# Kernel optimization log

Measured on AMD Instinct MI355X. Metric: run time of the kernel, lower is better.

The kernel has to match this reference:

```python
import jax, jax.numpy as jnp
import numpy as np

B, S, R = 8192, 256, 8192  # gas cells, species, reactions


def setup_inputs() -> dict:
    key = jax.random.key(0)
    ks = jax.random.split(key, 10)
    abundances = jax.random.uniform(ks[0], (B, S), jnp.float32, 1e-12, 1.0)
    temperature = jax.random.uniform(ks[1], (B,), jnp.float32, 10.0, 300.0)
    cr_rate = jax.random.uniform(ks[2], (B,), jnp.float32, 0.1, 10.0)
    fuv_rate = jax.random.uniform(ks[3], (B,), jnp.float32, 0.1, 10.0)
    time = jnp.zeros((B,), jnp.float32)  # unused by the RHS, kept for signature parity
    incidence = jax.random.normal(ks[4], (S, R), jnp.float32)  # stoichiometry matrix
    alpha = jax.random.uniform(ks[5], (R,), jnp.float32, 1e-12, 1e-9)
    beta = jax.random.normal(ks[6], (R,), jnp.float32) * 0.5
    gamma = jax.random.uniform(ks[7], (R,), jnp.float32, 0.0, 100.0)
    # species index or S (== out-of-bounds sentinel -> fill_value 1.0, i.e. <2 reactants)
    reactant_multipliers = jax.random.randint(ks[8], (R, 2), 0, S + 1, jnp.int32)
    rtype = jax.random.randint(ks[9], (R,), 0, 3, jnp.int32)  # 0: Arrhenius, 1: CR, 2: FUV
    return {
        'time': time, 'abundances': abundances, 'temperature': temperature,
        'cr_rate': cr_rate, 'fuv_rate': fuv_rate, 'incidence': incidence,
        'alpha': alpha, 'beta': beta, 'gamma': gamma,
        'reactant_multipliers': reactant_multipliers, 'rtype': rtype,
    }


def _get_rates(temperature, cr_rate, fuv_rate, alpha, beta, gamma, rtype):
    # JNetwork.get_rates: hstack of per-reaction rate terms -> (B, R)
    T = temperature[:, None]                                      # (B, 1)
    k_arr = alpha * jnp.exp(beta * jnp.log(T / 300.0) - gamma / T)  # Arrhenius
    k_cr = alpha * cr_rate[:, None]                               # cosmic-ray driven
    k_fuv = alpha * jnp.exp(-gamma) * fuv_rate[:, None]           # FUV photorate
    return jnp.where(rtype == 0, k_arr, jnp.where(rtype == 1, k_cr, k_fuv))


def reference(time, abundances, temperature, cr_rate, fuv_rate,
              incidence, alpha, beta, gamma, reactant_multipliers, rtype):
    rates = _get_rates(temperature, cr_rate, fuv_rate, alpha, beta, gamma, rtype)
    # multiply_rates_by_abundance: gather reactant abundances (mode='drop',
    # fill_value=1.0) and reduce with a product over the 2 reactant slots.
    ones_col = jnp.ones((abundances.shape[0], 1), abundances.dtype)
    ab_pad = jnp.concatenate([abundances, ones_col], axis=1)      # (B, S+1), col S == 1.0
    prod = ab_pad[:, reactant_multipliers[:, 0]] * ab_pad[:, reactant_multipliers[:, 1]]  # (B, R)
    flux = rates * prod                                           # (B, R)
    # incidence @ rates, batched: (S, R) x (B, R) -> (B, S)
    return jnp.einsum('sr,br->bs', incidence, flux)
```

## Files before the change

kernel.cpp:

```cpp
#include <hip/hip_runtime.h>
#include <stdint.h>

typedef __bf16 bf16;
typedef __bf16 bf16x8 __attribute__((ext_vector_type(8)));
typedef float  f32x4  __attribute__((ext_vector_type(4)));

#if __has_builtin(__builtin_amdgcn_exp2f)
#define EXP2F(x) __builtin_amdgcn_exp2f(x)
#else
#define EXP2F(x) exp2f(x)
#endif

#define LGKM_BARRIER()                                    \
  do {                                                    \
    asm volatile("s_waitcnt lgkmcnt(0)" ::: "memory");    \
    __builtin_amdgcn_s_barrier();                         \
  } while (0)

constexpr int Bn = 8192, Sn = 256, Rn = 8192;
constexpr int BM = 64, BK = 32, KP = 4;
constexpr int KLEN = Rn / KP;
constexpr int NC = KLEN / BK;

__global__ __launch_bounds__(256) void prep_all(
    const float* __restrict__ inc, bf16* __restrict__ incb,
    const float* __restrict__ alpha, const float* __restrict__ beta,
    const float* __restrict__ gam, const int* __restrict__ rm, const int* __restrict__ rtype,
    float4* __restrict__ params, const float* __restrict__ temp,
    const float* __restrict__ cr, const float* __restrict__ fuv, float4* __restrict__ perb) {
  __shared__ __align__(16) float row_lds[8192];
  __shared__ unsigned short perm_lds[8192];
  __shared__ int c0[256], c1[256], c2[256];
  const int g = blockIdx.x, t = threadIdx.x;

  int* rt = (int*)row_lds;
  {
    const int4* src = (const int4*)rtype;
    int4* dst = (int4*)rt;
#pragma unroll
    for (int i = 0; i < 8; ++i) dst[i * 256 + t] = src[i * 256 + t];
  }
  __syncthreads();

  int ty[32];
  int l0 = 0, l1 = 0, l2 = 0;
#pragma unroll
  for (int i = 0; i < 32; ++i) {
    int v = rt[i * 256 + t];
    ty[i] = v;
    l0 += (v == 0); l1 += (v == 1); l2 += (v == 2);
  }
  c0[t] = l0; c1[t] = l1; c2[t] = l2;
  __syncthreads();
  for (int off = 1; off < 256; off <<= 1) {
    int a = (t >= off) ? c0[t - off] : 0;
    int b = (t >= off) ? c1[t - off] : 0;
    int c = (t >= off) ? c2[t - off] : 0;
    __syncthreads();
    c0[t] += a; c1[t] += b; c2[t] += c;
    __syncthreads();
  }
  const int tot0 = c0[255], tot1 = c1[255];
  int o0 = c0[t] - l0;
  int o1 = tot0 + c1[t] - l1;
  int o2 = tot0 + tot1 + c2[t] - l2;
#pragma unroll
  for (int i = 0; i < 32; ++i) {
    int v = ty[i];
    int pos = (v == 0) ? o0++ : ((v == 1) ? o1++ : o2++);
    perm_lds[pos] = (unsigned short)(i * 256 + t);
  }
  __syncthreads();

  if (g < 32) {
    int p = g * 256 + t;
    int r = perm_lds[p];
    float a = alpha[r], be = beta[r], gm = gam[r];
    int tv = rt[r];
    int i0 = rm[2 * r], i1 = rm[2 * r + 1];
    float x, P = 0.0f, Q = 0.0f;
    if (tv == 0) { x = __log2f(a); P = be; Q = gm; }
    else if (tv == 1) { x = a; }
    else { x = a * expf(-gm); }
    uint32_t bits = (uint32_t)i0 | ((uint32_t)i1 << 10) | ((uint32_t)tv << 20);
    params[p] = make_float4(x, P, Q, __uint_as_float(bits));
  } else if (g < 64) {
    int b = (g - 32) * 256 + t;
    float T = temp[b];
    perb[b] = make_float4(__log2f(T * (1.0f / 300.0f)), 1.4426950408889634f / T,
                          cr[b], fuv[b]);
  }
  __syncthreads();

  {
    const float4* src = (const float4*)(inc + ((size_t)g << 13));
    float4* dst = (float4*)row_lds;
#pragma unroll
    for (int i = 0; i < 8; ++i) dst[i * 256 + t] = src[i * 256 + t];
  }
  __syncthreads();

  const unsigned short* pp = perm_lds + t * 32;
  bf16* outp = incb + ((size_t)t * 256 + g) * 32;
#pragma unroll
  for (int k8 = 0; k8 < 4; ++k8) {
    bf16x8 o;
#pragma unroll
    for (int i = 0; i < 8; ++i) o[i] = (bf16)row_lds[pp[k8 * 8 + i]];
    *(bf16x8*)(outp + k8 * 8) = o;
  }
}

__global__ __launch_bounds__(256, 2) void flux_gemm(
    const float* __restrict__ abund, const float4* __restrict__ perb,
    const float4* __restrict__ params, const bf16* __restrict__ incb,
    float* __restrict__ partial) {
  __shared__ bf16 ab_lds[257 * 64];
  __shared__ bf16 flux_lds[2][64 * BK];

  const int tid  = threadIdx.x;
  const int lane = tid & 63;
  const int w    = tid >> 6;
  const int ws   = __builtin_amdgcn_readfirstlane(w);
  const int x   = blockIdx.x & 7;
  const int jb  = blockIdx.x >> 3;
  const int kp  = x & 3;
  const int m0g = (jb * 2 + (x >> 2)) * BM;
  const int kstart = kp * KLEN;
  const int r16 = lane & 15, q = lane >> 4;
  const int sw16 = (r16 >> 1) & 3;
  const int fsw  = w ^ ((lane >> 1) & 3);

  auto load_params = [&](int chunk, float4* pr) {
    const float4* pw = params + kstart + chunk * BK + ws * 8;
#pragma unroll
    for (int j = 0; j < 8; ++j) pr[j] = pw[j];
  };

  float4 prE[8], prO[8];
  load_params(0, prE);

  {
    int bsub = tid >> 2;
    int scol = (tid & 3) * 64;
    const float* rowp = abund + (size_t)(m0g + bsub) * Sn + scol;
#pragma unroll
    for (int j = 0; j < 16; ++j) {
      float4 v = *(const float4*)(rowp + j * 4);
      int s = scol + j * 4;
      ab_lds[(s + 0) * 64 + bsub] = (bf16)v.x;
      ab_lds[(s + 1) * 64 + bsub] = (bf16)v.y;
      ab_lds[(s + 2) * 64 + bsub] = (bf16)v.z;
      ab_lds[(s + 3) * 64 + bsub] = (bf16)v.w;
    }
    if (tid < 64) ab_lds[256 * 64 + tid] = (bf16)1.0f;
  }

  float4 pb = perb[m0g + lane];
  const float l2t = pb.x, nitv = -pb.y, crv = pb.z, fuvv = pb.w;

  auto flux_tile = [&](int buf, const float4* pr) {
    uint32_t b0 = __builtin_amdgcn_readfirstlane(__float_as_uint(pr[0].w));
    uint32_t b7 = __builtin_amdgcn_readfirstlane(__float_as_uint(pr[7].w));
    uint32_t t0 = b0 >> 20, t7 = b7 >> 20;
    bf16x8 fv;
    if (t0 == 0 && t7 == 0) {
#pragma unroll
      for (int j = 0; j < 8; ++j) {
        uint32_t bits = __builtin_amdgcn_readfirstlane(__float_as_uint(pr[j].w));
        int i0 = (int)(bits & 1023), i1 = (int)((bits >> 10) & 1023);
        float a0 = (float)ab_lds[i0 * 64 + lane];
        float a1 = (float)ab_lds[i1 * 64 + lane];
        float v = EXP2F(fmaf(pr[j].y, l2t, fmaf(pr[j].z, nitv, pr[j].x)));
        fv[j] = (bf16)(v * (a0 * a1));
      }
    } else if (t0 == t7) {
      float mv = (t0 == 1) ? crv : fuvv;
#pragma unroll
      for (int j = 0; j < 8; ++j) {
        uint32_t bits = __builtin_amdgcn_readfirstlane(__float_as_uint(pr[j].w));
        int i0 = (int)(bits & 1023), i1 = (int)((bits >> 10) & 1023);
        float a0 = (float)ab_lds[i0 * 64 + lane];
        float a1 = (float)ab_lds[i1 * 64 + lane];
        fv[j] = (bf16)((pr[j].x * mv) * (a0 * a1));
      }
    } else {
#pragma unroll
      for (int j = 0; j < 8; ++j) {
        uint32_t bits = __builtin_amdgcn_readfirstlane(__float_as_uint(pr[j].w));
        int i0 = (int)(bits & 1023), i1 = (int)((bits >> 10) & 1023), ms = (int)(bits >> 20);
        float a0 = (float)ab_lds[i0 * 64 + lane];
        float a1 = (float)ab_lds[i1 * 64 + lane];
        float ve = EXP2F(fmaf(pr[j].y, l2t, fmaf(pr[j].z, nitv, pr[j].x)));
        float vm = pr[j].x * ((ms == 1) ? crv : fuvv);
        float v = (ms == 0) ? ve : vm;
        fv[j] = (bf16)(v * (a0 * a1));
      }
    }
    *(bf16x8*)(flux_lds[buf] + lane * BK + fsw * 8) = fv;
  };

  const bf16* bbase = incb + (size_t)(kstart / BK) * 8192 + (w * 64 + r16) * BK + q * 8;
  auto load_bfr = [&](int chunk, bf16x8* bfr) {
    const bf16* bp = bbase + (size_t)chunk * 8192;
#pragma unroll
    for (int nt = 0; nt < 4; ++nt)
      bfr[nt] = *(const bf16x8*)(bp + nt * (16 * BK));
  };

  auto do_mfma = [&](f32x4 (*acc)[4], const bf16x8* af, const bf16x8* bfr) {
    __builtin_amdgcn_s_setprio(1);
#pragma unroll
    for (int mt = 0; mt < 4; ++mt)
#pragma unroll
      for (int nt = 0; nt < 4; ++nt)
        acc[mt][nt] = __builtin_amdgcn_mfma_f32_16x16x32_bf16(af[mt], bfr[nt], acc[mt][nt], 0, 0, 0);
    __builtin_amdgcn_s_setprio(0);
  };

  __syncthreads();

  flux_tile(0, prE);

  bf16x8 bfrA[4], bfrB[4];
  load_params(1, prO);
  load_bfr(0, bfrA);

  f32x4 acc[4][4];
#pragma unroll
  for (int i = 0; i < 4; ++i)
#pragma unroll
    for (int j = 0; j < 4; ++j) acc[i][j] = (f32x4)0.0f;

  for (int c = 0; c < NC; c += 2) {
    LGKM_BARRIER();
    bf16x8 afA[4];
#pragma unroll
    for (int mt = 0; mt < 4; ++mt)
      afA[mt] = *(const bf16x8*)(flux_lds[0] + (mt * 16 + r16) * BK + (q ^ sw16) * 8);
    {
      const int cp = (c + 2 < NC) ? c + 2 : NC - 1;
      load_params(cp, prE);
    }
    load_bfr(c + 1, bfrB);
    flux_tile(1, prO);
    do_mfma(acc, afA, bfrA);

    LGKM_BARRIER();
    bf16x8 afB[4];
#pragma unroll
    for (int mt = 0; mt < 4; ++mt)
      afB[mt] = *(const bf16x8*)(flux_lds[1] + (mt * 16 + r16) * BK + (q ^ sw16) * 8);
    {
      const int cp = (c + 3 < NC) ? c + 3 : NC - 1;
      load_params(cp, prO);
    }
    {
      const int cp = (c + 2 < NC) ? c + 2 : NC - 1;
      load_bfr(cp, bfrA);
    }
    if (c + 2 < NC) flux_tile(0, prE);
    do_mfma(acc, afB, bfrB);
  }

  float* pout = partial + (size_t)kp * Bn * Sn;
#pragma unroll
  for (int mt = 0; mt < 4; ++mt)
#pragma unroll
    for (int nt = 0; nt < 4; ++nt) {
      int col = w * 64 + nt * 16 + r16;
      int row = m0g + mt * 16 + q * 4;
#pragma unroll
      for (int rg = 0; rg < 4; ++rg)
        pout[(size_t)(row + rg) * Sn + col] = acc[mt][nt][rg];
    }
}

__global__ __launch_bounds__(256) void reduce_k(const float* __restrict__ partial,
                                               float* __restrict__ out) {
  size_t i = ((size_t)blockIdx.x * 256 + threadIdx.x) * 4;
  constexpr size_t NS = (size_t)Bn * Sn;
  float4 a = *(const float4*)(partial + i);
  float4 b = *(const float4*)(partial + NS + i);
  float4 c = *(const float4*)(partial + 2 * NS + i);
  float4 d = *(const float4*)(partial + 3 * NS + i);
  float4 r;
  r.x = (a.x + b.x) + (c.x + d.x);
  r.y = (a.y + b.y) + (c.y + d.y);
  r.z = (a.z + b.z) + (c.z + d.z);
  r.w = (a.w + b.w) + (c.w + d.w);
  *(float4*)(out + i) = r;
}

extern "C" void kernel_launch(void* const* d_in, const int* in_sizes, int n_in,
                              void* d_out, int out_size, void* d_ws, size_t ws_size,
                              hipStream_t stream) {
  const float* abund = (const float*)d_in[1];
  const float* temp  = (const float*)d_in[2];
  const float* cr    = (const float*)d_in[3];
  const float* fuv   = (const float*)d_in[4];
  const float* inc   = (const float*)d_in[5];
  const float* alpha = (const float*)d_in[6];
  const float* beta  = (const float*)d_in[7];
  const float* gam   = (const float*)d_in[8];
  const int*   rm    = (const int*)d_in[9];
  const int*   rty   = (const int*)d_in[10];
  float* out = (float*)d_out;

  float4* params  = (float4*)d_ws;
  float4* perb    = params + Rn;
  bf16*   incb    = (bf16*)(perb + Bn);
  float*  partial = (float*)(incb + (size_t)Sn * Rn);

  prep_all<<<256, 256, 0, stream>>>(inc, incb, alpha, beta, gam, rm, rty,
                                    params, temp, cr, fuv, perb);
  flux_gemm<<<(Bn / BM) * KP, 256, 0, stream>>>(abund, perb, params, incb, partial);
  reduce_k<<<(Bn * Sn) / 1024, 256, 0, stream>>>(partial, out);
}
```

Measured before the change: 154.8 us.

## Double flux K-phase to 64 and restructure pipeline to one barrier per phase

Each pipeline phase now covers 64 reactions (two 32-wide sub-tiles) instead of 32. The loop uses a single barrier per phase, with a new XOR swizzle on the wider flux LDS tile. Params and incidence fragments are loaded inside each phase rather than prefetched one chunk ahead in registers. This halves barrier count and doubles MFMA work per sync, but drops the register-level prefetch of B fragments, so global-load latency may be less well hidden.

```diff
diff --git a/kernel.cpp b/kernel.cpp
--- a/kernel.cpp
+++ b/kernel.cpp
@@ -21,6 +21,8 @@
 constexpr int BM = 64, BK = 32, KP = 4;
 constexpr int KLEN = Rn / KP;
 constexpr int NC = KLEN / BK;
+constexpr int PH = 64;
+constexpr int NP = KLEN / PH;
 
 __global__ __launch_bounds__(256) void prep_all(
     const float* __restrict__ inc, bf16* __restrict__ incb,
@@ -116,7 +118,7 @@
     const float4* __restrict__ params, const bf16* __restrict__ incb,
     float* __restrict__ partial) {
   __shared__ bf16 ab_lds[257 * 64];
-  __shared__ bf16 flux_lds[2][64 * BK];
+  __shared__ bf16 flux_lds[2][64 * PH];
 
   const int tid  = threadIdx.x;
   const int lane = tid & 63;
@@ -128,17 +130,17 @@
   const int m0g = (jb * 2 + (x >> 2)) * BM;
   const int kstart = kp * KLEN;
   const int r16 = lane & 15, q = lane >> 4;
-  const int sw16 = (r16 >> 1) & 3;
-  const int fsw  = w ^ ((lane >> 1) & 3);
-
-  auto load_params = [&](int chunk, float4* pr) {
-    const float4* pw = params + kstart + chunk * BK + ws * 8;
+
+  auto load_params = [&](int ph, float4* pr) {
+    const float4* pw = params + kstart + ph * PH + ws * 8;
 #pragma unroll
     for (int j = 0; j < 8; ++j) pr[j] = pw[j];
+#pragma unroll
+    for (int j = 0; j < 8; ++j) pr[8 + j] = pw[32 + j];
   };
 
-  float4 prE[8], prO[8];
-  load_params(0, prE);
+  float4 prbuf[16];
+  load_params(0, prbuf);
 
   {
     int bsub = tid >> 2;
@@ -159,7 +161,7 @@
   float4 pb = perb[m0g + lane];
   const float l2t = pb.x, nitv = -pb.y, crv = pb.z, fuvv = pb.w;
 
-  auto flux_tile = [&](int buf, const float4* pr) {
+  auto flux_tile = [&](int buf, int sub, const float4* pr) {
     uint32_t b0 = __builtin_amdgcn_readfirstlane(__float_as_uint(pr[0].w));
     uint32_t b7 = __builtin_amdgcn_readfirstlane(__float_as_uint(pr[7].w));
     uint32_t t0 = b0 >> 20, t7 = b7 >> 20;
@@ -197,7 +199,7 @@
         fv[j] = (bf16)(v * (a0 * a1));
       }
     }
-    *(bf16x8*)(flux_lds[buf] + lane * BK + fsw * 8) = fv;
+    *(bf16x8*)(flux_lds[buf] + lane * PH + (((sub * 4 + ws) ^ (lane & 7)) << 3)) = fv;
   };
 
   const bf16* bbase = incb + (size_t)(kstart / BK) * 8192 + (w * 64 + r16) * BK + q * 8;
@@ -208,59 +210,51 @@
       bfr[nt] = *(const bf16x8*)(bp + nt * (16 * BK));
   };
 
-  auto do_mfma = [&](f32x4 (*acc)[4], const bf16x8* af, const bf16x8* bfr) {
+  __syncthreads();
+
+  flux_tile(0, 0, prbuf);
+  flux_tile(0, 1, prbuf + 8);
+
+  f32x4 acc[4][4];
+#pragma unroll
+  for (int i = 0; i < 4; ++i)
+#pragma unroll
+    for (int j = 0; j < 4; ++j) acc[i][j] = (f32x4)0.0f;
+
+  for (int ph = 0; ph < NP; ++ph) {
+    const int cur = ph & 1, nxt = cur ^ 1;
+    LGKM_BARRIER();
+
+    bf16x8 bfr[2][4];
+    load_bfr(ph * 2, bfr[0]);
+    load_bfr(ph * 2 + 1, bfr[1]);
+
+    bf16x8 af[2][4];
+#pragma unroll
+    for (int ks = 0; ks < 2; ++ks)
+#pragma unroll
+      for (int mt = 0; mt < 4; ++mt) {
+        int row = mt * 16 + r16;
+        af[ks][mt] = *(const bf16x8*)(flux_lds[cur] + row * PH +
+                                      ((((ks << 2) + q) ^ (row & 7)) << 3));
+      }
+
+    if (ph + 1 < NP) {
+      load_params(ph + 1, prbuf);
+      flux_tile(nxt, 0, prbuf);
+      flux_tile(nxt, 1, prbuf + 8);
+    }
+
     __builtin_amdgcn_s_setprio(1);
 #pragma unroll
-    for (int mt = 0; mt < 4; ++mt)
-#pragma unroll
-      for (int nt = 0; nt < 4; ++nt)
-        acc[mt][nt] = __builtin_amdgcn_mfma_f32_16x16x32_bf16(af[mt], bfr[nt], acc[mt][nt], 0, 0, 0);
+    for (int ks = 0; ks < 2; ++ks)
+#pragma unroll
+      for (int mt = 0; mt < 4; ++mt)
+#pragma unroll
+        for (int nt = 0; nt < 4; ++nt)
+          acc[mt][nt] = __builtin_amdgcn_mfma_f32_16x16x32_bf16(af[ks][mt], bfr[ks][nt],
+                                                                acc[mt][nt], 0, 0, 0);
     __builtin_amdgcn_s_setprio(0);
-  };
-
-  __syncthreads();
-
-  flux_tile(0, prE);
-
-  bf16x8 bfrA[4], bfrB[4];
-  load_params(1, prO);
-  load_bfr(0, bfrA);
-
-  f32x4 acc[4][4];
-#pragma unroll
-  for (int i = 0; i < 4; ++i)
-#pragma unroll
-    for (int j = 0; j < 4; ++j) acc[i][j] = (f32x4)0.0f;
-
-  for (int c = 0; c < NC; c += 2) {
-    LGKM_BARRIER();
-    bf16x8 afA[4];
-#pragma unroll
-    for (int mt = 0; mt < 4; ++mt)
-      afA[mt] = *(const bf16x8*)(flux_lds[0] + (mt * 16 + r16) * BK + (q ^ sw16) * 8);
-    {
-      const int cp = (c + 2 < NC) ? c + 2 : NC - 1;
-      load_params(cp, prE);
-    }
-    load_bfr(c + 1, bfrB);
-    flux_tile(1, prO);
-    do_mfma(acc, afA, bfrA);
-
-    LGKM_BARRIER();
-    bf16x8 afB[4];
-#pragma unroll
-    for (int mt = 0; mt < 4; ++mt)
-      afB[mt] = *(const bf16x8*)(flux_lds[1] + (mt * 16 + r16) * BK + (q ^ sw16) * 8);
-    {
-      const int cp = (c + 3 < NC) ? c + 3 : NC - 1;
-      load_params(cp, prO);
-    }
-    {
-      const int cp = (c + 2 < NC) ? c + 2 : NC - 1;
-      load_bfr(cp, bfrA);
-    }
-    if (c + 2 < NC) flux_tile(0, prE);
-    do_mfma(acc, afB, bfrB);
   }
 
   float* pout = partial + (size_t)kp * Bn * Sn;
```

After: 154.8 us (median of 2 runs). About the same (-0.0%).
